# Performance work log

Measured on AMD Instinct MI355X. Metric: run time of the kernel, lower is better.

## Reference

```python
import jax, jax.numpy as jnp
import numpy as np

# Config (matches init_kwargs)
B, C, H, W = 32, 128, 12, 1200   # z: (B, in_dim, H, W)
DIN = C * H                       # 1536
FIX = 768                         # get_multiple(DIN // 2, 6)
OV = 4                            # overlap
G = 6                             # num_vqs
D = OV * FIX // G                 # 512 per-group embedding size (all equal)
K = 1024                          # codebook_size
COMMIT = 0.25


def setup_inputs() -> dict:
    key = jax.random.key(0)
    k1, k2, k3, k4 = jax.random.split(key, 4)
    z = jax.random.normal(k1, (B, C, H, W), dtype=jnp.float32)
    w_down = jax.random.normal(k2, (FIX, DIN), dtype=jnp.float32) * 0.02
    w_up = jax.random.normal(k3, (DIN, FIX), dtype=jnp.float32) * 0.02
    embedding = jax.random.normal(k4, (G, D, K), dtype=jnp.float32)  # per-group (embedding_size, num_embedding)
    return {"z": z, "w_down": w_down, "w_up": w_up, "embedding": embedding}


def _quantize_group(zg, emb):
    # zg: (B, T, D), emb: (D, K)
    zf = zg.reshape(-1, D)
    # squared euclidean distance: |z|^2 - 2 z@E + |E|^2 -> (N, K)
    dist = (zf * zf).sum(1, keepdims=True) - 2.0 * (zf @ emb) + (emb * emb).sum(0, keepdims=True)
    idx = jnp.argmin(dist, axis=1)            # (N,)
    q = jnp.take(emb.T, idx, axis=0).reshape(zg.shape)
    # straight-through estimator (training mode)
    zq = zg + jax.lax.stop_gradient(q - zg)
    loss = COMMIT * jnp.mean((jax.lax.stop_gradient(zq) - zg) ** 2)
    return zq, loss


def reference(z, w_down, w_up, embedding):
    # pre_process: (B,C,H,W) -> permute(0,2,3,1) -> permute(0,2,3,1) -> (B, W, C*H)
    x = jnp.transpose(z, (0, 3, 1, 2)).reshape(B, W, DIN)  # (B, W, C, H) flattened
    x = x @ w_down.T                                       # proj_down -> (B, W, FIX)
    T = W // OV
    x = x.reshape(B, T, OV * FIX)                          # (B, T, 3072)
    # split into G contiguous groups of size D along last axis -> (G, B, T, D)
    xg = jnp.transpose(x.reshape(B, T, G, D), (2, 0, 1, 3))
    zq_g, losses = jax.vmap(_quantize_group)(xg, embedding)
    vq_loss = losses.sum() / G
    # concat groups back -> (B, T, G*D)
    zq = jnp.transpose(zq_g, (1, 2, 0, 3)).reshape(B, T, G * D)
    # post_process: un-overlap, proj_up, back to (B, C, H, W)
    zq = zq.reshape(B, W, FIX)
    zq = zq @ w_up.T                                       # (B, W, DIN)
    zq = zq.reshape(B, W, C, H)
    zq = jnp.transpose(zq, (0, 3, 1, 2))                   # (B, H, W, C)
    zq = jnp.transpose(zq, (0, 3, 1, 2))                   # dim==4 -> (B, C, H, W)
    return zq, vq_loss
```

## Files before the change

kernel.cpp:

```cpp
#include <hip/hip_runtime.h>

#define BB 32
#define CC 128
#define HH 12
#define WW 1200
#define DIN 1536
#define FIXD 768
#define OVL 4
#define GG 6
#define DD 512
#define KK 1024
#define TT 300
#define NV 9600
#define MROWS 38400

#define Y_OFF     0
#define ET_OFF    29491200
#define NORM_OFF  32636928
#define BEST_OFF  32643072
#define LOSS_OFF  32758272
#define ZN_OFF    32758336
#define UMIN_OFF  32815936
#define CNT_OFF   32873536
#define MAXN_OFF  32931136
#define LIST_OFF  32931200
#define YBF_OFF   36617600
#define EBF_OFF   51363200

#define BSWZ(c) ((c) + 4 * ((c) >> 5))

typedef __attribute__((ext_vector_type(8))) short bf16x8;
typedef __attribute__((ext_vector_type(4))) float f32x4;

static __device__ inline unsigned short f2bf(float x) {
    unsigned u = __float_as_uint(x);
    unsigned r = (u + 0x7fffu + ((u >> 16) & 1u)) >> 16;
    return (unsigned short)r;
}
static __device__ inline unsigned enc32(float s) {
    unsigned u = __float_as_uint(s);
    return (u & 0x80000000u) ? ~u : (u | 0x80000000u);
}

__global__ __launch_bounds__(256) void k_gemm_down(const float* __restrict__ z,
                                                   const float* __restrict__ w_down,
                                                   float* __restrict__ Y) {
    __shared__ float As[16][132];
    __shared__ float Bs[16][140];
    const int n0 = blockIdx.y * 128, f0 = blockIdx.x * 128;
    const int tid = threadIdx.x;
    const int arow = tid & 127;
    const int ak0 = tid >> 7;
    const int nA = n0 + arow;
    const int bA = nA / WW, wA = nA - bA * WW;
    const size_t zbase = (size_t)bA * (CC * HH * WW) + wA;
    const int bcol = tid >> 1, bq = tid & 1;
    const int bsc = BSWZ(bcol);
    const int trow = tid >> 4, tcol = tid & 15;
    const int bread = tcol * 8 + 4 * (tcol >> 2);
    float acc[8][8] = {};
    for (int kt = 0; kt < DIN; kt += 16) {
        #pragma unroll
        for (int i = 0; i < 8; i++) {
            const int kk = ak0 + i * 2;
            As[kk][arow] = z[zbase + (size_t)(kt + kk) * WW];
        }
        #pragma unroll
        for (int i = 0; i < 2; i++) {
            const int q = bq + i * 2;
            const float4 v = *(const float4*)&w_down[(size_t)(f0 + bcol) * DIN + kt + q * 4];
            Bs[q * 4 + 0][bsc] = v.x;
            Bs[q * 4 + 1][bsc] = v.y;
            Bs[q * 4 + 2][bsc] = v.z;
            Bs[q * 4 + 3][bsc] = v.w;
        }
        __syncthreads();
        #pragma unroll
        for (int k = 0; k < 16; k++) {
            float av[8], bv[8];
            *(float4*)&av[0] = *(const float4*)&As[k][trow * 8];
            *(float4*)&av[4] = *(const float4*)&As[k][trow * 8 + 4];
            *(float4*)&bv[0] = *(const float4*)&Bs[k][bread];
            *(float4*)&bv[4] = *(const float4*)&Bs[k][bread + 4];
            #pragma unroll
            for (int i = 0; i < 8; i++)
                #pragma unroll
                for (int j = 0; j < 8; j++)
                    acc[i][j] = fmaf(av[i], bv[j], acc[i][j]);
        }
        __syncthreads();
    }
    #pragma unroll
    for (int i = 0; i < 8; i++) {
        float4 o0, o1;
        o0.x = acc[i][0]; o0.y = acc[i][1]; o0.z = acc[i][2]; o0.w = acc[i][3];
        o1.x = acc[i][4]; o1.y = acc[i][5]; o1.z = acc[i][6]; o1.w = acc[i][7];
        float* yr = &Y[(size_t)(n0 + trow * 8 + i) * FIXD + f0 + tcol * 8];
        *(float4*)yr = o0;
        *(float4*)(yr + 4) = o1;
    }
}

__global__ __launch_bounds__(256) void k_transpose(const float* __restrict__ emb,
                                                   float* __restrict__ ET) {
    int i = blockIdx.x * 256 + threadIdx.x;
    if (i >= GG * KK * DD) return;
    int d = i & 511;
    int rem = i >> 9;
    int k = rem & 1023;
    int g = rem >> 10;
    ET[i] = emb[((g * DD + d) << 10) + k];
}

__global__ __launch_bounds__(64) void k_norms(const float* __restrict__ ET,
                                              float* __restrict__ norms,
                                              unsigned* __restrict__ maxnU) {
    const int code = blockIdx.x;
    const int lane = threadIdx.x;
    const float* row = ET + code * DD;
    double s = 0.0;
    #pragma unroll
    for (int r = 0; r < 8; r++) {
        float v = row[lane + r * 64];
        s += (double)v * (double)v;
    }
    #pragma unroll
    for (int off = 32; off; off >>= 1) s += __shfl_down(s, off);
    if (lane == 0) {
        const float nf = (float)s;
        norms[code] = nf;
        atomicMax(&maxnU[code >> 10], __float_as_uint(nf));
    }
}

__global__ __launch_bounds__(256) void k_ysplit(const float* __restrict__ Y,
                                                unsigned short* __restrict__ Ybf,
                                                float* __restrict__ znorm) {
    const int gv = blockIdx.x * 4 + (threadIdx.x >> 6);
    const int lane = threadIdx.x & 63;
    const int g = gv / NV, r = gv - g * NV;
    const int b = r / TT, t = r - b * TT;
    const int d0 = lane * 8;
    const int p = g * DD + d0;
    const int sg = p / FIXD, f = p - sg * FIXD;
    const float* yb = &Y[(size_t)((b * WW + t * OVL + sg) * FIXD + f)];
    const float4 y0 = *(const float4*)yb;
    const float4 y1 = *(const float4*)(yb + 4);
    unsigned short h[8];
    h[0] = f2bf(y0.x); h[1] = f2bf(y0.y); h[2] = f2bf(y0.z); h[3] = f2bf(y0.w);
    h[4] = f2bf(y1.x); h[5] = f2bf(y1.y); h[6] = f2bf(y1.z); h[7] = f2bf(y1.w);
    *(uint4*)&Ybf[(size_t)gv * DD + d0] = *(uint4*)&h[0];
    float s = 0.f;
    s = fmaf(y0.x, y0.x, s); s = fmaf(y0.y, y0.y, s);
    s = fmaf(y0.z, y0.z, s); s = fmaf(y0.w, y0.w, s);
    s = fmaf(y1.x, y1.x, s); s = fmaf(y1.y, y1.y, s);
    s = fmaf(y1.z, y1.z, s); s = fmaf(y1.w, y1.w, s);
    #pragma unroll
    for (int off = 32; off; off >>= 1) s += __shfl_down(s, off);
    if (lane == 0) znorm[gv] = s;
}

__global__ __launch_bounds__(256) void k_esplit(const float* __restrict__ ET,
                                                unsigned short* __restrict__ Ebf) {
    const size_t i8 = ((size_t)blockIdx.x * 256 + threadIdx.x) * 8;
    const float4 a = *(const float4*)&ET[i8];
    const float4 b = *(const float4*)&ET[i8 + 4];
    unsigned short h[8];
    h[0] = f2bf(a.x); h[1] = f2bf(a.y); h[2] = f2bf(a.z); h[3] = f2bf(a.w);
    h[4] = f2bf(b.x); h[5] = f2bf(b.y); h[6] = f2bf(b.z); h[7] = f2bf(b.w);
    *(uint4*)&Ebf[i8] = *(uint4*)&h[0];
}

template<int PHASE>
__global__ __launch_bounds__(256) void k_dist3(const unsigned short* __restrict__ Ybf,
                                               const unsigned short* __restrict__ Ebf,
                                               const float* __restrict__ norms,
                                               const float* __restrict__ znorm,
                                               const unsigned* __restrict__ maxnU,
                                               unsigned* __restrict__ umin,
                                               unsigned* __restrict__ cnt,
                                               unsigned* __restrict__ list_) {
    __shared__ unsigned short Ah[128][40], Bh[128][40];
    __shared__ float a1s[128], margs[128];
    const int vt = blockIdx.x;
    const int ct = blockIdx.y;
    const int g  = blockIdx.z;
    const int v0 = vt * 128, c0 = ct * 128;
    const int tid = threadIdx.x;
    const size_t ybase = ((size_t)g * NV + v0) * DD;
    const size_t ebase = ((size_t)g * KK + c0) * DD;
    const int srow = tid >> 1, sseg = (tid & 1) * 16;
    const int wv = tid >> 6, lane = tid & 63;
    const int wr = wv >> 1, wc = wv & 1;
    const int m0 = wr * 64, n0 = wc * 64;
    const int lr = lane & 15, lq = lane >> 4;

    if (PHASE == 2 && tid < 128) {
        const int gv = g * NV + v0 + tid;
        const unsigned u = umin[gv];
        const unsigned x = (u & 0x80000000u) ? (u & 0x7fffffffu) : ~u;
        a1s[tid] = __uint_as_float(x);
        margs[tid] = 0.032f * sqrtf(znorm[gv] * __uint_as_float(maxnU[g]));
    }

    f32x4 acc[4][4];
    #pragma unroll
    for (int i = 0; i < 4; i++)
        #pragma unroll
        for (int j = 0; j < 4; j++) acc[i][j] = (f32x4){0.f, 0.f, 0.f, 0.f};

    for (int kt = 0; kt < DD; kt += 32) {
        {
            const uint4 a0 = *(const uint4*)&Ybf[ybase + (size_t)srow * DD + kt + sseg];
            const uint4 a1 = *(const uint4*)&Ybf[ybase + (size_t)srow * DD + kt + sseg + 8];
            const uint4 b0 = *(const uint4*)&Ebf[ebase + (size_t)srow * DD + kt + sseg];
            const uint4 b1 = *(const uint4*)&Ebf[ebase + (size_t)srow * DD + kt + sseg + 8];
            *(uint4*)&Ah[srow][sseg]     = a0;
            *(uint4*)&Ah[srow][sseg + 8] = a1;
            *(uint4*)&Bh[srow][sseg]     = b0;
            *(uint4*)&Bh[srow][sseg + 8] = b1;
        }
        __syncthreads();
        bf16x8 ah[4], bh[4];
        #pragma unroll
        for (int i = 0; i < 4; i++) {
            ah[i] = *(bf16x8*)&Ah[m0 + i * 16 + lr][lq * 8];
            bh[i] = *(bf16x8*)&Bh[n0 + i * 16 + lr][lq * 8];
        }
        #pragma unroll
        for (int i = 0; i < 4; i++)
            #pragma unroll
            for (int j = 0; j < 4; j++)
                acc[i][j] = __builtin_amdgcn_mfma_f32_16x16x32_bf16(ah[i], bh[j], acc[i][j], 0, 0, 0);
        __syncthreads();
    }

    float nrmj[4];
    #pragma unroll
    for (int j = 0; j < 4; j++) nrmj[j] = norms[(g << 10) + c0 + n0 + j * 16 + lr];

    #pragma unroll
    for (int i = 0; i < 4; i++) {
        #pragma unroll
        for (int rr = 0; rr < 4; rr++) {
            const int row = m0 + i * 16 + lq * 4 + rr;
            if (PHASE == 1) {
                unsigned kb = 0xFFFFFFFFu;
                #pragma unroll
                for (int j = 0; j < 4; j++) {
                    const unsigned u = enc32(nrmj[j] - 2.0f * acc[i][j][rr]);
                    kb = (u < kb) ? u : kb;
                }
                #pragma unroll
                for (int off = 1; off < 16; off <<= 1) {
                    const unsigned o = __shfl_xor(kb, off);
                    kb = (o < kb) ? o : kb;
                }
                if (lr == 0) atomicMin(&umin[g * NV + v0 + row], kb);
            } else {
                const float thr = a1s[row] + margs[row];
                #pragma unroll
                for (int j = 0; j < 4; j++) {
                    const float sc = nrmj[j] - 2.0f * acc[i][j][rr];
                    if (sc <= thr) {
                        const int gv = g * NV + v0 + row;
                        const unsigned idx = atomicAdd(&cnt[gv], 1u);
                        if (idx < 64u)
                            list_[(size_t)gv * 64 + idx] = (unsigned)(c0 + n0 + j * 16 + lr);
                    }
                }
            }
        }
    }
}

__global__ __launch_bounds__(64) void k_rescore(const float* __restrict__ Y,
                                                const float* __restrict__ ET,
                                                const float* __restrict__ norms,
                                                const unsigned* __restrict__ cnt,
                                                const unsigned* __restrict__ list_,
                                                unsigned long long* __restrict__ best) {
    const int gv = blockIdx.x;
    const unsigned n = cnt[gv];
    if (n == 0u || n > 64u) return;
    const int lane = threadIdx.x;
    const int g = gv / NV, r = gv - g * NV;
    const int b = r / TT, t = r - b * TT;
    unsigned long long key = ~0ull;
    if (lane < (int)n) {
        const unsigned c = list_[(size_t)gv * 64 + lane];
        const float* erow = &ET[((size_t)((g << 10) + c)) * DD];
        float s = 0.f;
        for (int d4 = 0; d4 < 128; ++d4) {
            const int p = g * DD + d4 * 4;
            const int sg = p / FIXD, f = p - sg * FIXD;
            const float4 yv = *(const float4*)&Y[(size_t)((b * WW + t * OVL + sg) * FIXD + f)];
            const float4 ev = *(const float4*)&erow[d4 * 4];
            s = fmaf(yv.x, ev.x, s); s = fmaf(yv.y, ev.y, s);
            s = fmaf(yv.z, ev.z, s); s = fmaf(yv.w, ev.w, s);
        }
        const float sc = norms[(g << 10) + c] - 2.0f * s;
        key = ((unsigned long long)enc32(sc) << 32) | c;
    }
    #pragma unroll
    for (int off = 32; off; off >>= 1) {
        const unsigned long long o = __shfl_down(key, off);
        if (o < key) key = o;
    }
    if (lane == 0) best[gv] = key;
}

__global__ __launch_bounds__(256) void k_fallback(const float* __restrict__ Y,
                                                  const float* __restrict__ ET,
                                                  const float* __restrict__ norms,
                                                  const unsigned* __restrict__ cnt,
                                                  unsigned long long* __restrict__ best) {
    const int gv = blockIdx.x;
    if (cnt[gv] <= 64u) return;
    __shared__ float Yv[512];
    __shared__ unsigned long long red[256];
    const int tid = threadIdx.x;
    const int g = gv / NV, r = gv - g * NV;
    const int b = r / TT, t = r - b * TT;
    if (tid < 128) {
        const int p = g * DD + tid * 4;
        const int sg = p / FIXD, f = p - sg * FIXD;
        *(float4*)&Yv[tid * 4] = *(const float4*)&Y[(size_t)((b * WW + t * OVL + sg) * FIXD + f)];
    }
    __syncthreads();
    unsigned long long kb = ~0ull;
    for (int cc = 0; cc < 4; ++cc) {
        const int c = tid + cc * 256;
        const float* erow = &ET[((size_t)((g << 10) + c)) * DD];
        float s = 0.f;
        for (int d = 0; d < 512; ++d) s = fmaf(Yv[d], erow[d], s);
        const float sc = norms[(g << 10) + c] - 2.0f * s;
        const unsigned long long key = ((unsigned long long)enc32(sc) << 32) | (unsigned)c;
        if (key < kb) kb = key;
    }
    red[tid] = kb;
    __syncthreads();
    for (int off = 128; off; off >>= 1) {
        if (tid < off) { if (red[tid + off] < red[tid]) red[tid] = red[tid + off]; }
        __syncthreads();
    }
    if (tid == 0) best[gv] = red[0];
}

__global__ __launch_bounds__(256) void k_sumloss(const unsigned long long* __restrict__ best,
                                                 const float* __restrict__ znorm,
                                                 float* __restrict__ lossAcc) {
    const int v = blockIdx.x * 256 + threadIdx.x;
    const unsigned long long key = best[v];
    const unsigned u = (unsigned)(key >> 32);
    const unsigned x = (u & 0x80000000u) ? (u & 0x7fffffffu) : ~u;
    float s = __uint_as_float(x) + znorm[v];
    __shared__ float red[256];
    red[threadIdx.x] = s;
    __syncthreads();
    for (int off = 128; off; off >>= 1) {
        if (threadIdx.x < off) red[threadIdx.x] += red[threadIdx.x + off];
        __syncthreads();
    }
    if (threadIdx.x == 0) atomicAdd(lossAcc, red[0]);
}

__constant__ int SEG_G[8]  = {0, 1, 1, 2, 3, 4, 4, 5};
__constant__ int SEG_D0[8] = {0, 0, 256, 0, 0, 0, 256, 0};
__constant__ int SEG_L[8]  = {512, 256, 256, 512, 512, 256, 256, 512};
__constant__ int SEG_F0[8] = {0, 512, 0, 256, 0, 512, 0, 256};

__global__ __launch_bounds__(256) void k_table(const float* __restrict__ ET,
                                               const float* __restrict__ w_up,
                                               float* __restrict__ Tab) {
    __shared__ float As[16][68];
    __shared__ float Bs[16][140];
    const int bm = blockIdx.x;
    const int bn = blockIdx.y;
    const int seg = blockIdx.z;
    const int g = SEG_G[seg], d0 = SEG_D0[seg], len = SEG_L[seg], fb = SEG_F0[seg];
    const int tid = threadIdx.x;
    const int k0 = bm * 64, dout0 = bn * 128;
    const int arow = tid >> 2, aq = tid & 3;
    const int rbase = (tid >> 4) << 2;
    const int cgrp = tid & 15;
    const int bread = cgrp * 8 + 4 * (cgrp >> 2);
    const float* ETg = ET + (size_t)(g << 10) * DD;
    float acc[4][8] = {};
    for (int kt = 0; kt < len; kt += 16) {
        {
            const float4 v = *(const float4*)&ETg[(size_t)(k0 + arow) * DD + d0 + kt + aq * 4];
            As[aq * 4 + 0][arow] = v.x;
            As[aq * 4 + 1][arow] = v.y;
            As[aq * 4 + 2][arow] = v.z;
            As[aq * 4 + 3][arow] = v.w;
        }
        #pragma unroll
        for (int i = 0; i < 2; i++) {
            int fl = tid + i * 256;
            int col = fl >> 2, q = fl & 3;
            const int sc = BSWZ(col);
            const float4 v = *(const float4*)&w_up[(size_t)(dout0 + col) * FIXD + fb + kt + q * 4];
            Bs[q * 4 + 0][sc] = v.x;
            Bs[q * 4 + 1][sc] = v.y;
            Bs[q * 4 + 2][sc] = v.z;
            Bs[q * 4 + 3][sc] = v.w;
        }
        __syncthreads();
        #pragma unroll
        for (int k = 0; k < 16; k++) {
            const float4 a  = *(const float4*)&As[k][rbase];
            const float4 ba = *(const float4*)&Bs[k][bread];
            const float4 bb = *(const float4*)&Bs[k][bread + 4];
            const float av[4] = {a.x, a.y, a.z, a.w};
            const float bv[8] = {ba.x, ba.y, ba.z, ba.w, bb.x, bb.y, bb.z, bb.w};
            #pragma unroll
            for (int i = 0; i < 4; i++)
                #pragma unroll
                for (int j = 0; j < 8; j++)
                    acc[i][j] = fmaf(av[i], bv[j], acc[i][j]);
        }
        __syncthreads();
    }
    #pragma unroll
    for (int i = 0; i < 4; i++) {
        float4 o0, o1;
        o0.x = acc[i][0]; o0.y = acc[i][1]; o0.z = acc[i][2]; o0.w = acc[i][3];
        o1.x = acc[i][4]; o1.y = acc[i][5]; o1.z = acc[i][6]; o1.w = acc[i][7];
        float* tr = &Tab[(size_t)((seg << 10) + k0 + rbase + i) * DIN + dout0 + cgrp * 8];
        *(float4*)tr = o0;
        *(float4*)(tr + 4) = o1;
    }
}

__global__ __launch_bounds__(256) void k_scatter(const float* __restrict__ Tab,
                                                 const unsigned long long* __restrict__ best,
                                                 float* __restrict__ out) {
    __shared__ float Ls[64][65];
    const int dt = blockIdx.x;
    const int wt = blockIdx.y;
    const int b  = blockIdx.z;
    const int dout0 = dt * 64, w0 = wt * 64;
    const int wlim = (WW - w0 < 64) ? (WW - w0) : 64;
    const int tid = threadIdx.x;
    const int wi = tid >> 2, q = tid & 3;

    if (wi < wlim) {
        const int w = w0 + wi;
        const int s = w & 3;
        const int t = w >> 2;
        const int gEt[4] = {0, 1, 3, 4};
        const int gOt[4] = {1, 2, 4, 5};
        int ce = (int)(unsigned)best[gEt[s] * NV + b * TT + t];
        int co = (int)(unsigned)best[gOt[s] * NV + b * TT + t];
        size_t rowE = (size_t)(((2 * s) << 10) + ce) * DIN;
        size_t rowO = (size_t)(((2 * s + 1) << 10) + co) * DIN;
        #pragma unroll
        for (int rep = 0; rep < 4; rep++) {
            const int doff = rep * 16 + q * 4;
            const float4 a = *(const float4*)&Tab[rowE + dout0 + doff];
            const float4 c = *(const float4*)&Tab[rowO + dout0 + doff];
            Ls[wi][doff + 0] = a.x + c.x;
            Ls[wi][doff + 1] = a.y + c.y;
            Ls[wi][doff + 2] = a.z + c.z;
            Ls[wi][doff + 3] = a.w + c.w;
        }
    }
    __syncthreads();
    const size_t obase = (size_t)b * (CC * HH * WW) + (size_t)dout0 * WW + w0;
    #pragma unroll
    for (int i = 0; i < 16; i++) {
        int flat = tid + i * 256;
        int dr = flat >> 6, wj = flat & 63;
        if (wj < wlim) out[obase + (size_t)dr * WW + wj] = Ls[wj][dr];
    }
}

__global__ void k_finish(const float* __restrict__ lossAcc, float* __restrict__ out) {
    if (threadIdx.x == 0)
        out[58982400] = lossAcc[0] * (0.25f / 29491200.0f);
}

extern "C" void kernel_launch(void* const* d_in, const int* in_sizes, int n_in,
                              void* d_out, int out_size, void* d_ws, size_t ws_size,
                              hipStream_t stream) {
    const float* z      = (const float*)d_in[0];
    const float* w_down = (const float*)d_in[1];
    const float* w_up   = (const float*)d_in[2];
    const float* emb    = (const float*)d_in[3];
    float* out = (float*)d_out;

    float* ws    = (float*)d_ws;
    float* Y     = ws + Y_OFF;
    float* Tab   = ws + Y_OFF;
    float* ET    = ws + ET_OFF;
    float* norms = ws + NORM_OFF;
    unsigned long long* best = (unsigned long long*)(ws + BEST_OFF);
    float* lossA = ws + LOSS_OFF;
    float* znorm = ws + ZN_OFF;
    unsigned* umin  = (unsigned*)(ws + UMIN_OFF);
    unsigned* cnt   = (unsigned*)(ws + CNT_OFF);
    unsigned* maxnU = (unsigned*)(ws + MAXN_OFF);
    unsigned* list_ = (unsigned*)(ws + LIST_OFF);
    unsigned short* Ybf = (unsigned short*)(ws + YBF_OFF);
    unsigned short* Ebf = (unsigned short*)(ws + EBF_OFF);

    hipMemsetAsync(best, 0xFF, (size_t)GG * NV * sizeof(unsigned long long), stream);
    hipMemsetAsync(umin, 0xFF, (size_t)GG * NV * sizeof(unsigned), stream);
    hipMemsetAsync(cnt, 0, (size_t)GG * NV * sizeof(unsigned), stream);
    hipMemsetAsync(maxnU, 0, 64, stream);
    hipMemsetAsync(lossA, 0, sizeof(float), stream);

    dim3 gdown(6, 300);
    k_gemm_down<<<gdown, 256, 0, stream>>>(z, w_down, Y);

    k_transpose<<<(GG * KK * DD + 255) / 256, 256, 0, stream>>>(emb, ET);
    k_norms<<<GG * KK, 64, 0, stream>>>(ET, norms, maxnU);

    k_ysplit<<<GG * NV / 4, 256, 0, stream>>>(Y, Ybf, znorm);
    k_esplit<<<GG * KK * DD / (256 * 8), 256, 0, stream>>>(ET, Ebf);

    dim3 gdist(75, 8, GG);
    k_dist3<1><<<gdist, 256, 0, stream>>>(Ybf, Ebf, norms, znorm, maxnU, umin, cnt, list_);
    k_dist3<2><<<gdist, 256, 0, stream>>>(Ybf, Ebf, norms, znorm, maxnU, umin, cnt, list_);

    k_rescore<<<GG * NV, 64, 0, stream>>>(Y, ET, norms, cnt, list_, best);
    k_fallback<<<GG * NV, 256, 0, stream>>>(Y, ET, norms, cnt, best);

    k_sumloss<<<225, 256, 0, stream>>>(best, znorm, lossA);

    dim3 gtab(16, 12, 8);
    k_table<<<gtab, 256, 0, stream>>>(ET, w_up, Tab);

    dim3 gsc(24, 19, 32);
    k_scatter<<<gsc, 256, 0, stream>>>(Tab, best, out);

    k_finish<<<1, 64, 0, stream>>>(lossA, out);
}
```

Measured before the change: 2.001 ms.

## Double-buffer down-projection GEMM and fuse bf16 split and norm into epilogue

The fp32 down-projection GEMM now uses double-buffered shared memory with register prefetch, so the next k-tile's global loads overlap the current tile's FMAs and one barrier per iteration is removed. Its epilogue also writes the bf16 copy of Y and accumulates per-vector squared norms with atomics, which removes the separate k_ysplit pass that re-read Y. The distance kernel grid is reordered so consecutive blocks cover codebook tiles of the same row tile. The cost is doubled LDS use, more registers in the GEMM, an extra memset, and atomic float adds, which make znorm summation order nondeterministic.

```diff
diff --git a/kernel.cpp b/kernel.cpp
--- a/kernel.cpp
+++ b/kernel.cpp
@@ -44,9 +44,11 @@
 
 __global__ __launch_bounds__(256) void k_gemm_down(const float* __restrict__ z,
                                                    const float* __restrict__ w_down,
-                                                   float* __restrict__ Y) {
-    __shared__ float As[16][132];
-    __shared__ float Bs[16][140];
+                                                   float* __restrict__ Y,
+                                                   unsigned short* __restrict__ Ybf,
+                                                   float* __restrict__ znorm) {
+    __shared__ float As[2][16][132];
+    __shared__ float Bs[2][16][140];
     const int n0 = blockIdx.y * 128, f0 = blockIdx.x * 128;
     const int tid = threadIdx.x;
     const int arow = tid & 127;
@@ -59,45 +61,95 @@
     const int trow = tid >> 4, tcol = tid & 15;
     const int bread = tcol * 8 + 4 * (tcol >> 2);
     float acc[8][8] = {};
-    for (int kt = 0; kt < DIN; kt += 16) {
-        #pragma unroll
-        for (int i = 0; i < 8; i++) {
-            const int kk = ak0 + i * 2;
-            As[kk][arow] = z[zbase + (size_t)(kt + kk) * WW];
-        }
-        #pragma unroll
-        for (int i = 0; i < 2; i++) {
-            const int q = bq + i * 2;
-            const float4 v = *(const float4*)&w_down[(size_t)(f0 + bcol) * DIN + kt + q * 4];
-            Bs[q * 4 + 0][bsc] = v.x;
-            Bs[q * 4 + 1][bsc] = v.y;
-            Bs[q * 4 + 2][bsc] = v.z;
-            Bs[q * 4 + 3][bsc] = v.w;
-        }
-        __syncthreads();
+    float pa[8];
+    float4 pb[2];
+
+    #pragma unroll
+    for (int i = 0; i < 8; i++) pa[i] = z[zbase + (size_t)(ak0 + 2 * i) * WW];
+    #pragma unroll
+    for (int i = 0; i < 2; i++)
+        pb[i] = *(const float4*)&w_down[(size_t)(f0 + bcol) * DIN + (bq + 2 * i) * 4];
+    #pragma unroll
+    for (int i = 0; i < 8; i++) As[0][ak0 + 2 * i][arow] = pa[i];
+    #pragma unroll
+    for (int i = 0; i < 2; i++) {
+        const int q = bq + 2 * i;
+        Bs[0][q * 4 + 0][bsc] = pb[i].x;
+        Bs[0][q * 4 + 1][bsc] = pb[i].y;
+        Bs[0][q * 4 + 2][bsc] = pb[i].z;
+        Bs[0][q * 4 + 3][bsc] = pb[i].w;
+    }
+    __syncthreads();
+
+    for (int it = 0; it < 96; ++it) {
+        const int cur = it & 1;
+        if (it + 1 < 96) {
+            const int kt = (it + 1) * 16;
+            #pragma unroll
+            for (int i = 0; i < 8; i++)
+                pa[i] = z[zbase + (size_t)(kt + ak0 + 2 * i) * WW];
+            #pragma unroll
+            for (int i = 0; i < 2; i++)
+                pb[i] = *(const float4*)&w_down[(size_t)(f0 + bcol) * DIN + kt + (bq + 2 * i) * 4];
+        }
         #pragma unroll
         for (int k = 0; k < 16; k++) {
             float av[8], bv[8];
-            *(float4*)&av[0] = *(const float4*)&As[k][trow * 8];
-            *(float4*)&av[4] = *(const float4*)&As[k][trow * 8 + 4];
-            *(float4*)&bv[0] = *(const float4*)&Bs[k][bread];
-            *(float4*)&bv[4] = *(const float4*)&Bs[k][bread + 4];
+            *(float4*)&av[0] = *(const float4*)&As[cur][k][trow * 8];
+            *(float4*)&av[4] = *(const float4*)&As[cur][k][trow * 8 + 4];
+            *(float4*)&bv[0] = *(const float4*)&Bs[cur][k][bread];
+            *(float4*)&bv[4] = *(const float4*)&Bs[cur][k][bread + 4];
             #pragma unroll
             for (int i = 0; i < 8; i++)
                 #pragma unroll
                 for (int j = 0; j < 8; j++)
                     acc[i][j] = fmaf(av[i], bv[j], acc[i][j]);
         }
-        __syncthreads();
-    }
+        if (it + 1 < 96) {
+            const int nxt = cur ^ 1;
+            #pragma unroll
+            for (int i = 0; i < 8; i++) As[nxt][ak0 + 2 * i][arow] = pa[i];
+            #pragma unroll
+            for (int i = 0; i < 2; i++) {
+                const int q = bq + 2 * i;
+                Bs[nxt][q * 4 + 0][bsc] = pb[i].x;
+                Bs[nxt][q * 4 + 1][bsc] = pb[i].y;
+                Bs[nxt][q * 4 + 2][bsc] = pb[i].z;
+                Bs[nxt][q * 4 + 3][bsc] = pb[i].w;
+            }
+        }
+        __syncthreads();
+    }
+
     #pragma unroll
     for (int i = 0; i < 8; i++) {
+        const int n = n0 + trow * 8 + i;
+        const int fb = f0 + tcol * 8;
         float4 o0, o1;
         o0.x = acc[i][0]; o0.y = acc[i][1]; o0.z = acc[i][2]; o0.w = acc[i][3];
         o1.x = acc[i][4]; o1.y = acc[i][5]; o1.z = acc[i][6]; o1.w = acc[i][7];
-        float* yr = &Y[(size_t)(n0 + trow * 8 + i) * FIXD + f0 + tcol * 8];
+        float* yr = &Y[(size_t)n * FIXD + fb];
         *(float4*)yr = o0;
         *(float4*)(yr + 4) = o1;
+        const int b = n / WW, w = n - b * WW;
+        const int t = w >> 2, s = w & 3;
+        const int p = s * FIXD + fb;
+        const int g = p >> 9, d = p & 511;
+        const int gv = g * NV + b * TT + t;
+        unsigned short h[8];
+        h[0] = f2bf(o0.x); h[1] = f2bf(o0.y); h[2] = f2bf(o0.z); h[3] = f2bf(o0.w);
+        h[4] = f2bf(o1.x); h[5] = f2bf(o1.y); h[6] = f2bf(o1.z); h[7] = f2bf(o1.w);
+        *(uint4*)&Ybf[(size_t)gv * DD + d] = *(uint4*)&h[0];
+        float s2 = 0.f;
+        s2 = fmaf(o0.x, o0.x, s2); s2 = fmaf(o0.y, o0.y, s2);
+        s2 = fmaf(o0.z, o0.z, s2); s2 = fmaf(o0.w, o0.w, s2);
+        s2 = fmaf(o1.x, o1.x, s2); s2 = fmaf(o1.y, o1.y, s2);
+        s2 = fmaf(o1.z, o1.z, s2); s2 = fmaf(o1.w, o1.w, s2);
+        s2 += __shfl_xor(s2, 1);
+        s2 += __shfl_xor(s2, 2);
+        s2 += __shfl_xor(s2, 4);
+        s2 += __shfl_xor(s2, 8);
+        if (tcol == 0) atomicAdd(&znorm[gv], s2);
     }
 }
 
@@ -131,33 +183,6 @@
         norms[code] = nf;
         atomicMax(&maxnU[code >> 10], __float_as_uint(nf));
     }
-}
-
-__global__ __launch_bounds__(256) void k_ysplit(const float* __restrict__ Y,
-                                                unsigned short* __restrict__ Ybf,
-                                                float* __restrict__ znorm) {
-    const int gv = blockIdx.x * 4 + (threadIdx.x >> 6);
-    const int lane = threadIdx.x & 63;
-    const int g = gv / NV, r = gv - g * NV;
-    const int b = r / TT, t = r - b * TT;
-    const int d0 = lane * 8;
-    const int p = g * DD + d0;
-    const int sg = p / FIXD, f = p - sg * FIXD;
-    const float* yb = &Y[(size_t)((b * WW + t * OVL + sg) * FIXD + f)];
-    const float4 y0 = *(const float4*)yb;
-    const float4 y1 = *(const float4*)(yb + 4);
-    unsigned short h[8];
-    h[0] = f2bf(y0.x); h[1] = f2bf(y0.y); h[2] = f2bf(y0.z); h[3] = f2bf(y0.w);
-    h[4] = f2bf(y1.x); h[5] = f2bf(y1.y); h[6] = f2bf(y1.z); h[7] = f2bf(y1.w);
-    *(uint4*)&Ybf[(size_t)gv * DD + d0] = *(uint4*)&h[0];
-    float s = 0.f;
-    s = fmaf(y0.x, y0.x, s); s = fmaf(y0.y, y0.y, s);
-    s = fmaf(y0.z, y0.z, s); s = fmaf(y0.w, y0.w, s);
-    s = fmaf(y1.x, y1.x, s); s = fmaf(y1.y, y1.y, s);
-    s = fmaf(y1.z, y1.z, s); s = fmaf(y1.w, y1.w, s);
-    #pragma unroll
-    for (int off = 32; off; off >>= 1) s += __shfl_down(s, off);
-    if (lane == 0) znorm[gv] = s;
 }
 
 __global__ __launch_bounds__(256) void k_esplit(const float* __restrict__ ET,
@@ -182,8 +207,8 @@
                                                unsigned* __restrict__ list_) {
     __shared__ unsigned short Ah[128][40], Bh[128][40];
     __shared__ float a1s[128], margs[128];
-    const int vt = blockIdx.x;
-    const int ct = blockIdx.y;
+    const int ct = blockIdx.x;
+    const int vt = blockIdx.y;
     const int g  = blockIdx.z;
     const int v0 = vt * 128, c0 = ct * 128;
     const int tid = threadIdx.x;
@@ -508,19 +533,19 @@
     hipMemsetAsync(best, 0xFF, (size_t)GG * NV * sizeof(unsigned long long), stream);
     hipMemsetAsync(umin, 0xFF, (size_t)GG * NV * sizeof(unsigned), stream);
     hipMemsetAsync(cnt, 0, (size_t)GG * NV * sizeof(unsigned), stream);
+    hipMemsetAsync(znorm, 0, (size_t)GG * NV * sizeof(float), stream);
     hipMemsetAsync(maxnU, 0, 64, stream);
     hipMemsetAsync(lossA, 0, sizeof(float), stream);
 
     dim3 gdown(6, 300);
-    k_gemm_down<<<gdown, 256, 0, stream>>>(z, w_down, Y);
+    k_gemm_down<<<gdown, 256, 0, stream>>>(z, w_down, Y, Ybf, znorm);
 
     k_transpose<<<(GG * KK * DD + 255) / 256, 256, 0, stream>>>(emb, ET);
     k_norms<<<GG * KK, 64, 0, stream>>>(ET, norms, maxnU);
 
-    k_ysplit<<<GG * NV / 4, 256, 0, stream>>>(Y, Ybf, znorm);
     k_esplit<<<GG * KK * DD / (256 * 8), 256, 0, stream>>>(ET, Ebf);
 
-    dim3 gdist(75, 8, GG);
+    dim3 gdist(8, 75, GG);
     k_dist3<1><<<gdist, 256, 0, stream>>>(Ybf, Ebf, norms, znorm, maxnU, umin, cnt, list_);
     k_dist3<2><<<gdist, 256, 0, stream>>>(Ybf, Ebf, norms, znorm, maxnU, umin, cnt, list_);
 
```

Measured after the change: 2.544 ms. 27.1% more time.
